# Performance work log

Hardware: AMD Instinct MI355X
Metric: run time of the kernel (lower is better)

Reference implementation:

```python
import jax, jax.numpy as jnp
import numpy as np

N_NODES = 100000


def gcn_conv(x, W, b, src, dst, ew, n):
    """PyG GCNConv with edge_weight: add self-loops (weight 1), symmetric norm,
    linear transform, scatter-add aggregation, bias."""
    h = x @ W                                   # [N, F_out]
    # degree includes the self-loop weight of 1 per node
    deg = jnp.zeros((n,), dtype=x.dtype).at[dst].add(ew) + 1.0
    dinv = jax.lax.rsqrt(deg)                   # deg > 0 always (self-loop)
    norm = dinv[src] * ew * dinv[dst]           # [E]
    agg = jax.ops.segment_sum(h[src] * norm[:, None], dst, num_segments=n)
    # self-loop contribution: norm_ii = dinv[i]^2 * 1
    agg = agg + h * (dinv * dinv)[:, None]
    return agg + b


def setup_inputs() -> dict:
    key = jax.random.key(0)
    ks = jax.random.split(key, 9)
    N, E, F_in, F_h, F_out = N_NODES, 1600000, 128, 64, 10
    x = jax.random.normal(ks[0], (N, F_in), dtype=jnp.float32)
    edge_index = jax.random.randint(ks[1], (2, E), 0, N, dtype=jnp.int64)
    edge_weight = jax.random.uniform(ks[2], (E,), dtype=jnp.float32)
    def glorot(k, fi, fo):
        s = jnp.sqrt(6.0 / (fi + fo))
        return jax.random.uniform(k, (fi, fo), minval=-s, maxval=s, dtype=jnp.float32)
    return {
        "x": x,
        "edge_index": edge_index,
        "edge_weight": edge_weight,
        "W1": glorot(ks[3], F_in, F_h), "b1": jnp.zeros((F_h,), jnp.float32),
        "W2": glorot(ks[4], F_h, F_h), "b2": jnp.zeros((F_h,), jnp.float32),
        "Wfc": glorot(ks[5], F_h, F_out), "bfc": jnp.zeros((F_out,), jnp.float32),
    }


def reference(x, edge_index, edge_weight, W1, b1, W2, b2, Wfc, bfc):
    n = x.shape[0]
    src, dst = edge_index[0], edge_index[1]
    h = gcn_conv(x, W1, b1, src, dst, edge_weight, n)
    h = jax.nn.relu(h)
    h = gcn_conv(h, W2, b2, src, dst, edge_weight, n)
    h = jax.nn.relu(h)
    return h @ Wfc + bfc
```

## Files before the change

### kernel.cpp

```cpp
#include <hip/hip_runtime.h>

static constexpr int F_IN  = 128;
static constexpr int F_H   = 64;
static constexpr int F_OUT = 10;

static constexpr int NPB_SHIFT = 9;
static constexpr int NPB = 1 << NPB_SHIFT;
static constexpr int MAXC = 256;
static constexpr int EPB = 2048;

__device__ __forceinline__ unsigned short f2bf(float f) {
    unsigned u = __float_as_uint(f);
    return (unsigned short)((u + 0x7fff + ((u >> 16) & 1)) >> 16);
}
__device__ __forceinline__ float bf_lo(unsigned u) { return __uint_as_float(u << 16); }
__device__ __forceinline__ float bf_hi(unsigned u) { return __uint_as_float(u & 0xffff0000u); }

__global__ __launch_bounds__(64) void k_detect(const unsigned long long* __restrict__ u,
                                               int* __restrict__ flag) {
    unsigned long long v = u[threadIdx.x];
    int hz = ((v >> 32) == 0ull) ? 1 : 0;
    int all64 = __all(hz);
    if (threadIdx.x == 0) flag[0] = all64;
}

__device__ __forceinline__ int load_idx(const void* ein, bool f64, long i) {
    return f64 ? (int)((const long long*)ein)[i] : ((const int*)ein)[i];
}

__global__ __launch_bounds__(256) void k_part1(const void* __restrict__ ein,
                                               const float* __restrict__ ew,
                                               const int* __restrict__ flag,
                                               int* __restrict__ gcur,
                                               unsigned long long* __restrict__ packed,
                                               int E, int NC, int cap) {
    __shared__ int lcnt[MAXC];
    __shared__ int lofs[MAXC];
    int tid = threadIdx.x;
    if (tid < NC) lcnt[tid] = 0;
    __syncthreads();
    bool f = flag[0];
    int base = blockIdx.x * EPB;
#pragma unroll
    for (int j = 0; j < EPB / 256; ++j) {
        int e = base + j * 256 + tid;
        if (e < E) {
            int d = load_idx(ein, f, (long)E + e);
            atomicAdd(&lcnt[d >> NPB_SHIFT], 1);
        }
    }
    __syncthreads();
    if (tid < NC) {
        int c = lcnt[tid];
        lofs[tid] = c ? atomicAdd(&gcur[tid], c) : 0;
        lcnt[tid] = 0;
    }
    __syncthreads();
#pragma unroll
    for (int j = 0; j < EPB / 256; ++j) {
        int e = base + j * 256 + tid;
        if (e < E) {
            int s = load_idx(ein, f, e);
            int d = load_idx(ein, f, (long)E + e);
            unsigned int wb = __float_as_uint(ew[e]);
            int b = d >> NPB_SHIFT;
            int pos = lofs[b] + atomicAdd(&lcnt[b], 1);
            if (pos < cap) {
                unsigned long long u = (unsigned long long)wb
                                     | ((unsigned long long)(unsigned)s << 32)
                                     | ((unsigned long long)(unsigned)(d & (NPB - 1)) << 49);
                packed[(long)b * cap + pos] = u;
            }
        }
    }
}

__global__ __launch_bounds__(256) void k_chist(const unsigned long long* __restrict__ packed,
                                               const int* __restrict__ gcur,
                                               int* __restrict__ rp,
                                               int* __restrict__ pbt,
                                               float* __restrict__ dinv,
                                               int N, int cap) {
    __shared__ int   lc[NPB];
    __shared__ float ld[NPB];
    __shared__ int   sm[256];
    int b = blockIdx.x, tid = threadIdx.x;
#pragma unroll
    for (int i = tid; i < NPB; i += 256) { lc[i] = 0; ld[i] = 0.0f; }
    __syncthreads();
    int cnt = gcur[b];
    const unsigned long long* pk = packed + (long)b * cap;
    for (int p = tid; p < cnt; p += 256) {
        unsigned long long u = pk[p];
        int dl = (int)(u >> 49);
        atomicAdd(&lc[dl], 1);
        atomicAdd(&ld[dl], __uint_as_float((unsigned int)u));
    }
    __syncthreads();
    int c0 = lc[tid * 2], c1 = lc[tid * 2 + 1];
    int p0 = (c0 + 15) & ~15, p1 = (c1 + 15) & ~15;
    int s = p0 + p1;
    sm[tid] = s;
    __syncthreads();
    for (int off = 1; off < 256; off <<= 1) {
        int v = 0;
        if (tid >= off) v = sm[tid - off];
        __syncthreads();
        sm[tid] += v;
        __syncthreads();
    }
    int excl = sm[tid] - s;
    int n0 = b << NPB_SHIFT;
    int node0 = n0 + tid * 2, node1 = node0 + 1;
    if (node0 < N) {
        rp[node0]   = excl;
        dinv[node0] = rsqrtf(ld[tid * 2] + 1.0f);
    }
    if (node1 < N) {
        rp[node1]   = excl + p0;
        dinv[node1] = rsqrtf(ld[tid * 2 + 1] + 1.0f);
    }
    if (tid == 255) pbt[b] = sm[255];
}

__global__ __launch_bounds__(256) void k_scanP(const int* __restrict__ pbt,
                                               int* __restrict__ pbase,
                                               int* __restrict__ rp, int NC, int N) {
    __shared__ int sm[256];
    int tid = threadIdx.x;
    int c = (tid < NC) ? pbt[tid] : 0;
    sm[tid] = c;
    __syncthreads();
    for (int off = 1; off < 256; off <<= 1) {
        int v = 0;
        if (tid >= off) v = sm[tid - off];
        __syncthreads();
        sm[tid] += v;
        __syncthreads();
    }
    if (tid < NC) pbase[tid] = sm[tid] - c;
    if (tid == 255) rp[N] = sm[255];
}

__global__ __launch_bounds__(256) void k_rpfix(int* __restrict__ rp,
                                               const int* __restrict__ pbase, int N) {
    int i = blockIdx.x * 256 + threadIdx.x;
    if (i < N) rp[i] += pbase[i >> NPB_SHIFT];
}

__global__ __launch_bounds__(256) void k_cscatter(const unsigned long long* __restrict__ packed,
                                                  const int* __restrict__ gcur,
                                                  const int* __restrict__ rp,
                                                  const float* __restrict__ dinv,
                                                  uint2* __restrict__ recs,
                                                  int N, int cap) {
    __shared__ int   cur[NPB];
    __shared__ float dd[NPB];
    int b = blockIdx.x, tid = threadIdx.x;
    int n0 = b << NPB_SHIFT;
#pragma unroll
    for (int i = tid; i < NPB; i += 256) {
        int node = n0 + i;
        cur[i] = (node < N) ? rp[node]   : 0;
        dd[i]  = (node < N) ? dinv[node] : 0.0f;
    }
    __syncthreads();
    int cnt = gcur[b];
    const unsigned long long* pk = packed + (long)b * cap;
    for (int p = tid; p < cnt; p += 256) {
        unsigned long long u = pk[p];
        int dl = (int)(u >> 49);
        int s  = (int)((u >> 32) & 0x1FFFF);
        float w = __uint_as_float((unsigned int)u);
        int pos = atomicAdd(&cur[dl], 1);
        uint2 r;
        r.x = (unsigned)(s << 7);
        r.y = __float_as_uint(dinv[s] * w * dd[dl]);
        recs[pos] = r;
    }
    __syncthreads();
    for (int i = tid; i < NPB; i += 256) {
        int node = n0 + i;
        if (node < N) {
            int end = rp[node + 1];
            for (int p = cur[i]; p < end; ++p) recs[p] = make_uint2(0u, 0u);
        }
    }
}

template <int K>
__global__ __launch_bounds__(256) void k_gemm(const float* __restrict__ A,
                                              const float* __restrict__ W,
                                              unsigned short* __restrict__ Cb, int M) {
    __shared__ float As[64][68];
    __shared__ float Ws[64][64];
    int tid = threadIdx.x;
    int tx = tid & 15, ty = tid >> 4;
    int rb = blockIdx.x * 64;
    float acc[4][4] = {};
    for (int kc = 0; kc < K; kc += 64) {
        __syncthreads();
        for (int e = tid * 4; e < 64 * 64; e += 1024) {
            int r = e >> 6, k = e & 63;
            int gr = rb + r;
            float4 v = make_float4(0.f, 0.f, 0.f, 0.f);
            if (gr < M) v = *(const float4*)&A[(long)gr * K + kc + k];
            *(float4*)&As[r][k] = v;
        }
        for (int e = tid * 4; e < 64 * 64; e += 1024) {
            int r = e >> 6, k = e & 63;
            *(float4*)&Ws[r][k] = *(const float4*)&W[(long)(kc + r) * 64 + k];
        }
        __syncthreads();
#pragma unroll 16
        for (int k = 0; k < 64; ++k) {
            float a0 = As[ty * 4 + 0][k];
            float a1 = As[ty * 4 + 1][k];
            float a2 = As[ty * 4 + 2][k];
            float a3 = As[ty * 4 + 3][k];
            float4 b = *(float4*)&Ws[k][tx * 4];
            acc[0][0] = fmaf(a0, b.x, acc[0][0]); acc[0][1] = fmaf(a0, b.y, acc[0][1]);
            acc[0][2] = fmaf(a0, b.z, acc[0][2]); acc[0][3] = fmaf(a0, b.w, acc[0][3]);
            acc[1][0] = fmaf(a1, b.x, acc[1][0]); acc[1][1] = fmaf(a1, b.y, acc[1][1]);
            acc[1][2] = fmaf(a1, b.z, acc[1][2]); acc[1][3] = fmaf(a1, b.w, acc[1][3]);
            acc[2][0] = fmaf(a2, b.x, acc[2][0]); acc[2][1] = fmaf(a2, b.y, acc[2][1]);
            acc[2][2] = fmaf(a2, b.z, acc[2][2]); acc[2][3] = fmaf(a2, b.w, acc[2][3]);
            acc[3][0] = fmaf(a3, b.x, acc[3][0]); acc[3][1] = fmaf(a3, b.y, acc[3][1]);
            acc[3][2] = fmaf(a3, b.z, acc[3][2]); acc[3][3] = fmaf(a3, b.w, acc[3][3]);
        }
    }
#pragma unroll
    for (int j = 0; j < 4; ++j) {
        int gr = rb + ty * 4 + j;
        if (gr < M) {
            ushort4 v;
            v.x = f2bf(acc[j][0]); v.y = f2bf(acc[j][1]);
            v.z = f2bf(acc[j][2]); v.w = f2bf(acc[j][3]);
            *(ushort4*)&Cb[(long)gr * 64 + tx * 4] = v;
        }
    }
}

__global__ __launch_bounds__(256, 4) void k_agg(const unsigned short* __restrict__ hb,
                                                const int* __restrict__ rp,
                                                const uint2* __restrict__ recs,
                                                const float* __restrict__ dinv,
                                                const float* __restrict__ bias,
                                                float* __restrict__ out, int N) {
    int wid  = (blockIdx.x * 256 + threadIdx.x) >> 6;
    int lane = threadIdx.x & 63;
    int fg   = lane & 15;
    int es   = lane >> 4;
    if (wid >= N) return;
    int fg8 = fg * 8;
    const char* hbase = (const char*)hb;
    int p0 = rp[wid], p1 = rp[wid + 1];
    float a0 = 0.f, a1 = 0.f, a2 = 0.f, a3 = 0.f;
    for (int pb = p0 + es * 4; pb < p1; pb += 16) {
        uint4 r01 = *(const uint4*)&recs[pb];
        uint4 r23 = *(const uint4*)&recs[pb + 2];
        uint2 h0 = *(const uint2*)(hbase + r01.x + fg8);
        uint2 h1 = *(const uint2*)(hbase + r01.z + fg8);
        uint2 h2 = *(const uint2*)(hbase + r23.x + fg8);
        uint2 h3 = *(const uint2*)(hbase + r23.z + fg8);
        float w0 = __uint_as_float(r01.y), w1 = __uint_as_float(r01.w);
        float w2 = __uint_as_float(r23.y), w3 = __uint_as_float(r23.w);
        a0 = fmaf(w0, bf_lo(h0.x), a0); a1 = fmaf(w0, bf_hi(h0.x), a1);
        a2 = fmaf(w0, bf_lo(h0.y), a2); a3 = fmaf(w0, bf_hi(h0.y), a3);
        a0 = fmaf(w1, bf_lo(h1.x), a0); a1 = fmaf(w1, bf_hi(h1.x), a1);
        a2 = fmaf(w1, bf_lo(h1.y), a2); a3 = fmaf(w1, bf_hi(h1.y), a3);
        a0 = fmaf(w2, bf_lo(h2.x), a0); a1 = fmaf(w2, bf_hi(h2.x), a1);
        a2 = fmaf(w2, bf_lo(h2.y), a2); a3 = fmaf(w2, bf_hi(h2.y), a3);
        a0 = fmaf(w3, bf_lo(h3.x), a0); a1 = fmaf(w3, bf_hi(h3.x), a1);
        a2 = fmaf(w3, bf_lo(h3.y), a2); a3 = fmaf(w3, bf_hi(h3.y), a3);
    }
#pragma unroll
    for (int m = 16; m <= 32; m <<= 1) {
        a0 += __shfl_xor(a0, m);
        a1 += __shfl_xor(a1, m);
        a2 += __shfl_xor(a2, m);
        a3 += __shfl_xor(a3, m);
    }
    float di  = dinv[wid];
    float di2 = di * di;
    uint2 hs = *(const uint2*)(hbase + ((long)wid << 7) + fg8);
    float4 bv = *(const float4*)&bias[fg * 4];
    a0 = fmaf(bf_lo(hs.x), di2, a0 + bv.x);
    a1 = fmaf(bf_hi(hs.x), di2, a1 + bv.y);
    a2 = fmaf(bf_lo(hs.y), di2, a2 + bv.z);
    a3 = fmaf(bf_hi(hs.y), di2, a3 + bv.w);
    if (es == 0) {
        float4 r = make_float4(fmaxf(a0, 0.f), fmaxf(a1, 0.f),
                               fmaxf(a2, 0.f), fmaxf(a3, 0.f));
        *(float4*)&out[(long)wid * 64 + fg * 4] = r;
    }
}

__global__ __launch_bounds__(256) void k_fc(const float* __restrict__ h,
                                            const float* __restrict__ W,
                                            const float* __restrict__ b,
                                            float* __restrict__ out, int N) {
    __shared__ float Ws[64 * 10];
    __shared__ float bs[16];
    int tid = threadIdx.x;
    for (int e = tid; e < 64 * 10; e += 256) Ws[e] = W[e];
    if (tid < 10) bs[tid] = b[tid];
    __syncthreads();
    int i = blockIdx.x * 256 + tid;
    if (i >= N) return;
    float acc[10];
#pragma unroll
    for (int j = 0; j < 10; ++j) acc[j] = bs[j];
    const float4* row = (const float4*)&h[(long)i * 64];
#pragma unroll
    for (int c = 0; c < 16; ++c) {
        float4 a = row[c];
#pragma unroll
        for (int j = 0; j < 10; ++j) {
            acc[j] = fmaf(a.x, Ws[(4 * c + 0) * 10 + j], acc[j]);
            acc[j] = fmaf(a.y, Ws[(4 * c + 1) * 10 + j], acc[j]);
            acc[j] = fmaf(a.z, Ws[(4 * c + 2) * 10 + j], acc[j]);
            acc[j] = fmaf(a.w, Ws[(4 * c + 3) * 10 + j], acc[j]);
        }
    }
#pragma unroll
    for (int j = 0; j < 10; ++j) out[(long)i * 10 + j] = acc[j];
}

extern "C" void kernel_launch(void* const* d_in, const int* in_sizes, int n_in,
                              void* d_out, int out_size, void* d_ws, size_t ws_size,
                              hipStream_t stream) {
    const float* x    = (const float*)d_in[0];
    const void*  eidx = d_in[1];
    const float* ew   = (const float*)d_in[2];
    const float* W1   = (const float*)d_in[3];
    const float* b1   = (const float*)d_in[4];
    const float* W2   = (const float*)d_in[5];
    const float* b2   = (const float*)d_in[6];
    const float* Wfc  = (const float*)d_in[7];
    const float* bfc  = (const float*)d_in[8];
    float* out = (float*)d_out;

    const int N  = in_sizes[0] / F_IN;
    const int E  = in_sizes[2];
    const int NC = (N + NPB - 1) >> NPB_SHIFT;
    const int cap = E / NC + E / (8 * NC) + 1024;

    char* w = (char*)d_ws;
    size_t off = 0;
    auto alloc = [&](size_t bytes) {
        void* p = w + off;
        off += (bytes + 255) & ~(size_t)255;
        return p;
    };
    float* dinv  = (float*)alloc((size_t)N * 4);
    int*   rp    = (int*)alloc((size_t)(N + 1) * 4);
    int*   flag  = (int*)alloc(256);
    int*   gcur  = (int*)alloc((size_t)MAXC * 4);
    int*   pbt   = (int*)alloc((size_t)MAXC * 4);
    int*   pbase = (int*)alloc((size_t)MAXC * 4);
    unsigned long long* packed =
        (unsigned long long*)alloc((size_t)NC * cap * 8);
    uint2* recs  = (uint2*)alloc(((size_t)E + 15u * (size_t)N + 64) * 8);
    unsigned short* h1b = (unsigned short*)alloc((size_t)N * F_H * 2);
    float* g1    = (float*)alloc((size_t)N * F_H * 4);
    unsigned short* h2b = h1b;
    float* g2    = g1;
    (void)ws_size;

    hipMemsetAsync(gcur, 0, (size_t)NC * 4, stream);

    const int PB = (E + EPB - 1) / EPB;

    k_detect<<<1, 64, 0, stream>>>((const unsigned long long*)eidx, flag);
    k_part1<<<PB, 256, 0, stream>>>(eidx, ew, flag, gcur, packed, E, NC, cap);
    k_chist<<<NC, 256, 0, stream>>>(packed, gcur, rp, pbt, dinv, N, cap);
    k_scanP<<<1, 256, 0, stream>>>(pbt, pbase, rp, NC, N);
    k_rpfix<<<(N + 255) / 256, 256, 0, stream>>>(rp, pbase, N);
    k_cscatter<<<NC, 256, 0, stream>>>(packed, gcur, rp, dinv, recs, N, cap);

    const int GB = (N + 63) / 64;
    k_gemm<F_IN><<<GB, 256, 0, stream>>>(x, W1, h1b, N);
    k_agg<<<(N + 3) / 4, 256, 0, stream>>>(h1b, rp, recs, dinv, b1, g1, N);
    k_gemm<F_H><<<GB, 256, 0, stream>>>(g1, W2, h2b, N);
    k_agg<<<(N + 3) / 4, 256, 0, stream>>>(h2b, rp, recs, dinv, b2, g2, N);
    k_fc<<<(N + 255) / 256, 256, 0, stream>>>(g2, Wfc, bfc, out, N);
}
```

Before: 228.1 us.

## Retile GEMM to 128-row blocks with 8x4 per-thread tile and XOR-swizzled shared memory

The dense transform kernel now processes 128 rows per block with a 32-wide K chunk, and each thread computes an 8x4 output tile. A operands are read from shared memory as float4 vectors instead of scalars. An XOR swizzle on the A tile avoids bank conflicts on those vector reads. This raises register reuse and cuts LDS instructions per FMA, at the cost of more registers, fewer blocks and more K-loop iterations with syncs.

```diff
diff --git a/kernel.cpp b/kernel.cpp
--- a/kernel.cpp
+++ b/kernel.cpp
@@ -192,50 +192,68 @@
 __global__ __launch_bounds__(256) void k_gemm(const float* __restrict__ A,
                                               const float* __restrict__ W,
                                               unsigned short* __restrict__ Cb, int M) {
-    __shared__ float As[64][68];
-    __shared__ float Ws[64][64];
+    __shared__ float As[128][32];
+    __shared__ float Ws[32][64];
     int tid = threadIdx.x;
-    int tx = tid & 15, ty = tid >> 4;
-    int rb = blockIdx.x * 64;
-    float acc[4][4] = {};
-    for (int kc = 0; kc < K; kc += 64) {
-        __syncthreads();
-        for (int e = tid * 4; e < 64 * 64; e += 1024) {
-            int r = e >> 6, k = e & 63;
+    int tx = tid & 15;
+    int ty = tid >> 4;
+    int rb = blockIdx.x * 128;
+    float acc[8][4] = {};
+    for (int kc = 0; kc < K; kc += 32) {
+        __syncthreads();
+#pragma unroll
+        for (int i = 0; i < 4; ++i) {
+            int e = tid + i * 256;
+            int r = e >> 3, g = e & 7;
             int gr = rb + r;
             float4 v = make_float4(0.f, 0.f, 0.f, 0.f);
-            if (gr < M) v = *(const float4*)&A[(long)gr * K + kc + k];
-            *(float4*)&As[r][k] = v;
-        }
-        for (int e = tid * 4; e < 64 * 64; e += 1024) {
-            int r = e >> 6, k = e & 63;
-            *(float4*)&Ws[r][k] = *(const float4*)&W[(long)(kc + r) * 64 + k];
-        }
-        __syncthreads();
-#pragma unroll 16
-        for (int k = 0; k < 64; ++k) {
-            float a0 = As[ty * 4 + 0][k];
-            float a1 = As[ty * 4 + 1][k];
-            float a2 = As[ty * 4 + 2][k];
-            float a3 = As[ty * 4 + 3][k];
-            float4 b = *(float4*)&Ws[k][tx * 4];
-            acc[0][0] = fmaf(a0, b.x, acc[0][0]); acc[0][1] = fmaf(a0, b.y, acc[0][1]);
-            acc[0][2] = fmaf(a0, b.z, acc[0][2]); acc[0][3] = fmaf(a0, b.w, acc[0][3]);
-            acc[1][0] = fmaf(a1, b.x, acc[1][0]); acc[1][1] = fmaf(a1, b.y, acc[1][1]);
-            acc[1][2] = fmaf(a1, b.z, acc[1][2]); acc[1][3] = fmaf(a1, b.w, acc[1][3]);
-            acc[2][0] = fmaf(a2, b.x, acc[2][0]); acc[2][1] = fmaf(a2, b.y, acc[2][1]);
-            acc[2][2] = fmaf(a2, b.z, acc[2][2]); acc[2][3] = fmaf(a2, b.w, acc[2][3]);
-            acc[3][0] = fmaf(a3, b.x, acc[3][0]); acc[3][1] = fmaf(a3, b.y, acc[3][1]);
-            acc[3][2] = fmaf(a3, b.z, acc[3][2]); acc[3][3] = fmaf(a3, b.w, acc[3][3]);
-        }
-    }
-#pragma unroll
-    for (int j = 0; j < 4; ++j) {
-        int gr = rb + ty * 4 + j;
+            if (gr < M) v = *(const float4*)&A[(long)gr * K + kc + g * 4];
+            int gs = g ^ ((r >> 3) & 7);
+            *(float4*)&As[r][gs * 4] = v;
+        }
+#pragma unroll
+        for (int i = 0; i < 2; ++i) {
+            int e = tid + i * 256;
+            int k = e >> 4, n4 = e & 15;
+            *(float4*)&Ws[k][n4 * 4] = *(const float4*)&W[(long)(kc + k) * 64 + n4 * 4];
+        }
+        __syncthreads();
+#pragma unroll
+        for (int g = 0; g < 8; ++g) {
+            float4 b0 = *(const float4*)&Ws[g * 4 + 0][tx * 4];
+            float4 b1 = *(const float4*)&Ws[g * 4 + 1][tx * 4];
+            float4 b2 = *(const float4*)&Ws[g * 4 + 2][tx * 4];
+            float4 b3 = *(const float4*)&Ws[g * 4 + 3][tx * 4];
+            int gs = (g ^ (ty & 7)) * 4;
+#pragma unroll
+            for (int rr = 0; rr < 8; ++rr) {
+                float4 a = *(const float4*)&As[ty * 8 + rr][gs];
+                acc[rr][0] = fmaf(a.x, b0.x, acc[rr][0]);
+                acc[rr][1] = fmaf(a.x, b0.y, acc[rr][1]);
+                acc[rr][2] = fmaf(a.x, b0.z, acc[rr][2]);
+                acc[rr][3] = fmaf(a.x, b0.w, acc[rr][3]);
+                acc[rr][0] = fmaf(a.y, b1.x, acc[rr][0]);
+                acc[rr][1] = fmaf(a.y, b1.y, acc[rr][1]);
+                acc[rr][2] = fmaf(a.y, b1.z, acc[rr][2]);
+                acc[rr][3] = fmaf(a.y, b1.w, acc[rr][3]);
+                acc[rr][0] = fmaf(a.z, b2.x, acc[rr][0]);
+                acc[rr][1] = fmaf(a.z, b2.y, acc[rr][1]);
+                acc[rr][2] = fmaf(a.z, b2.z, acc[rr][2]);
+                acc[rr][3] = fmaf(a.z, b2.w, acc[rr][3]);
+                acc[rr][0] = fmaf(a.w, b3.x, acc[rr][0]);
+                acc[rr][1] = fmaf(a.w, b3.y, acc[rr][1]);
+                acc[rr][2] = fmaf(a.w, b3.z, acc[rr][2]);
+                acc[rr][3] = fmaf(a.w, b3.w, acc[rr][3]);
+            }
+        }
+    }
+#pragma unroll
+    for (int rr = 0; rr < 8; ++rr) {
+        int gr = rb + ty * 8 + rr;
         if (gr < M) {
             ushort4 v;
-            v.x = f2bf(acc[j][0]); v.y = f2bf(acc[j][1]);
-            v.z = f2bf(acc[j][2]); v.w = f2bf(acc[j][3]);
+            v.x = f2bf(acc[rr][0]); v.y = f2bf(acc[rr][1]);
+            v.z = f2bf(acc[rr][2]); v.w = f2bf(acc[rr][3]);
             *(ushort4*)&Cb[(long)gr * 64 + tx * 4] = v;
         }
     }
@@ -379,7 +397,7 @@
     k_rpfix<<<(N + 255) / 256, 256, 0, stream>>>(rp, pbase, N);
     k_cscatter<<<NC, 256, 0, stream>>>(packed, gcur, rp, dinv, recs, N, cap);
 
-    const int GB = (N + 63) / 64;
+    const int GB = (N + 127) / 128;
     k_gemm<F_IN><<<GB, 256, 0, stream>>>(x, W1, h1b, N);
     k_agg<<<(N + 3) / 4, 256, 0, stream>>>(h1b, rp, recs, dinv, b1, g1, N);
     k_gemm<F_H><<<GB, 256, 0, stream>>>(g1, W2, h2b, N);
```

Result: faster. 220.5 us (-3.3%).
